# Kernel tuning notes

Hardware: AMD Instinct MI355X
Metric: run time of the kernel (lower is better)

## Reference

```python
import jax, jax.numpy as jnp
import numpy as np

NUM_NODES = 100000
D_IN = 64
D_OUT = 64
NUM_EDGES = 1200000


def setup_inputs() -> dict:
    key = jax.random.key(0)
    k1, k2, k3, k4 = jax.random.split(key, 4)
    features = jax.random.normal(k1, (NUM_NODES, D_IN), dtype=jnp.float32)
    edge_index = jax.random.randint(k2, (2, NUM_EDGES), 0, NUM_NODES, dtype=jnp.int64)
    # Linear(input_dim*2 -> output_dim) parameters
    W = jax.random.normal(k3, (2 * D_IN, D_OUT), dtype=jnp.float32) / np.sqrt(2 * D_IN)
    b = jax.random.normal(k4, (D_OUT,), dtype=jnp.float32) * 0.01
    return {"features": features, "edge_index": edge_index, "W": W, "b": b}


def reference(features, edge_index, W, b):
    num_nodes = features.shape[0]
    src, dst = edge_index[0], edge_index[1]
    # gather source-node features for every edge: [E, D]
    src_feats = features[src]
    # segment-sum into destination nodes (mean aggregation)
    neigh_sum = jax.ops.segment_sum(src_feats, dst, num_segments=num_nodes)
    degree = jax.ops.segment_sum(jnp.ones_like(dst, dtype=features.dtype), dst,
                                 num_segments=num_nodes)
    degree = jnp.clip(degree, 1.0)
    neigh_mean = neigh_sum / degree[:, None]
    # concat self + neighbor features, then linear (dropout = identity in eval)
    combined = jnp.concatenate([features, neigh_mean], axis=-1)
    return combined @ W + b
```

## Files before the change

kernel.cpp:

```cpp
#include <hip/hip_runtime.h>
#include <hip/hip_fp8.h>

#define N_NODES 100000
#define D 64
#define N_EDGES 1200000
#define NCB 391
#define NBLK 256
#define PAD 16
#define CHUNK ((N_EDGES + NBLK - 1) / NBLK)

typedef __attribute__((ext_vector_type(8))) short short8v;
typedef __attribute__((ext_vector_type(4))) float f32x4;

__device__ __forceinline__ unsigned short f2bf(float x) {
    unsigned int b = __float_as_uint(x);
    b += 0x7FFFu + ((b >> 16) & 1u);
    return (unsigned short)(b >> 16);
}
__device__ __forceinline__ unsigned char ftofp8(float x) {
    __hip_fp8_e4m3 q(x);
    return (unsigned char)q.__x;
}
#if __has_builtin(__builtin_amdgcn_cvt_f32_fp8)
#define F8D(w, s) __builtin_amdgcn_cvt_f32_fp8((w), (s))
#else
__device__ __forceinline__ float f8dec(unsigned int w, unsigned int s) {
    __hip_fp8_e4m3 q; q.__x = (unsigned char)(w >> (8 * s));
    return (float)q;
}
#define F8D(w, s) f8dec((w), (s))
#endif

__global__ __launch_bounds__(256) void bin_hist(
    const int* __restrict__ eidx, int* __restrict__ hist, int* __restrict__ totP,
    const float* __restrict__ feat, unsigned char* __restrict__ f8b,
    const float* __restrict__ W, ushort* __restrict__ wb)
{
    __shared__ int h[NCB];
    for (int i = threadIdx.x; i < NCB; i += 256) h[i] = 0;
    __syncthreads();
    const int blk = blockIdx.x;

    if (blk < 32) {
        int g  = blk * 256 + threadIdx.x;
        int j  = g & 7;
        int l  = (g >> 3) & 63;
        int c4 = (g >> 9) & 3;
        int tt = g >> 11;
        int k   = 32 * tt + ((l >> 4) << 3) + j;
        int col = 16 * c4 + (l & 15);
        wb[g] = f2bf(W[k * 64 + col]);
    }

    const int beg = blk * CHUNK;
    const int end = min(beg + CHUNK, N_EDGES);
    for (int e = beg + threadIdx.x; e < end; e += 256)
        atomicAdd(&h[eidx[N_EDGES + e] >> 8], 1);

    const int total4 = N_NODES * D / 4;
    for (int i = blk * 256 + threadIdx.x; i < total4; i += NBLK * 256) {
        float4 v = ((const float4*)feat)[i];
        uchar4 o;
        o.x = ftofp8(v.x); o.y = ftofp8(v.y); o.z = ftofp8(v.z); o.w = ftofp8(v.w);
        ((uchar4*)f8b)[i] = o;
    }

    __syncthreads();
    for (int i = threadIdx.x; i < NCB; i += 256) {
        int v = h[i];
        hist[blk * NCB + i] = v;
        if (v) atomicAdd(&totP[i * PAD], v);
    }
}

__global__ __launch_bounds__(256) void rstart(
    const int* __restrict__ totP, const int* __restrict__ hist,
    int* __restrict__ boff, int* __restrict__ runstart, int* __restrict__ offs)
{
    __shared__ int red[256];
    __shared__ int pfx[256];
    __shared__ int bo_s;

    const int tid = threadIdx.x;
    const int i   = blockIdx.x;

    int p = 0;
    for (int j = tid; j < i; j += 256) p += totP[j * PAD];
    red[tid] = p;
    __syncthreads();
    for (int off = 128; off > 0; off >>= 1) {
        if (tid < off) red[tid] += red[tid + off];
        __syncthreads();
    }
    if (tid == 0) {
        bo_s = red[0];
        boff[i] = red[0];
        if (i == 0) { boff[NCB] = N_EDGES; offs[N_NODES] = N_EDGES; }
    }
    __syncthreads();

    int v = hist[tid * NCB + i];
    pfx[tid] = v;
    __syncthreads();
    for (int off = 1; off < 256; off <<= 1) {
        int x = (tid >= off) ? pfx[tid - off] : 0;
        __syncthreads();
        pfx[tid] += x;
        __syncthreads();
    }
    runstart[tid * NCB + i] = bo_s + pfx[tid] - v;
}

__global__ __launch_bounds__(256) void bin_fill(
    const int* __restrict__ eidx, const int* __restrict__ runstart,
    unsigned int* __restrict__ pairs)
{
    __shared__ int lcur[NCB];
    const int blk = blockIdx.x;
    for (int i = threadIdx.x; i < NCB; i += 256) lcur[i] = runstart[blk * NCB + i];
    __syncthreads();
    const int beg = blk * CHUNK;
    const int end = min(beg + CHUNK, N_EDGES);
    for (int e = beg + threadIdx.x; e < end; e += 256) {
        int src = eidx[e];
        int dst = eidx[N_EDGES + e];
        int pos = atomicAdd(&lcur[dst >> 8], 1);
        pairs[pos] = ((unsigned int)src << 8) | (unsigned int)(dst & 255);
    }
}

__global__ __launch_bounds__(256) void fine_sort(
    const unsigned int* __restrict__ pairs,
    const int* __restrict__ boff,
    int* __restrict__ offs,
    int* __restrict__ csr)
{
    __shared__ int cnt[256];
    __shared__ int pfx[256];
    __shared__ int lcur[256];

    const int tid = threadIdx.x;
    const int b   = blockIdx.x;
    const int beg = boff[b];
    const int end = boff[b + 1];

    cnt[tid] = 0;
    __syncthreads();
    for (int j = beg + tid; j < end; j += 256)
        atomicAdd(&cnt[pairs[j] & 255], 1);
    __syncthreads();

    int v = cnt[tid];
    pfx[tid] = v;
    __syncthreads();
    for (int off = 1; off < 256; off <<= 1) {
        int x = (tid >= off) ? pfx[tid - off] : 0;
        __syncthreads();
        pfx[tid] += x;
        __syncthreads();
    }
    int ex = pfx[tid] - v;
    lcur[tid] = ex;
    int gn = b * 256 + tid;
    if (gn < N_NODES) offs[gn] = beg + ex;
    __syncthreads();

    for (int j = beg + tid; j < end; j += 256) {
        unsigned int p = pairs[j];
        int pos = beg + atomicAdd(&lcur[p & 255], 1);
        csr[pos] = (int)(p >> 8);
    }
}

#define MROW 72
#define D8X(sel) (((F8D(w0.x,sel)+F8D(w1.x,sel))+(F8D(w2.x,sel)+F8D(w3.x,sel))) \
               + ((F8D(w4.x,sel)+F8D(w5.x,sel))+(F8D(w6.x,sel)+F8D(w7.x,sel))))
#define D8Y(sel) (((F8D(w0.y,sel)+F8D(w1.y,sel))+(F8D(w2.y,sel)+F8D(w3.y,sel))) \
               + ((F8D(w4.y,sel)+F8D(w5.y,sel))+(F8D(w6.y,sel)+F8D(w7.y,sel))))
#define D4X(sel) ((F8D(w0.x,sel)+F8D(w1.x,sel))+(F8D(w2.x,sel)+F8D(w3.x,sel)))
#define D4Y(sel) ((F8D(w0.y,sel)+F8D(w1.y,sel))+(F8D(w2.y,sel)+F8D(w3.y,sel)))
__global__ __launch_bounds__(256) void agg_gemm(
    const unsigned char* __restrict__ f8b,
    const float* __restrict__ feat,
    const int* __restrict__ offs,
    const int* __restrict__ csr,
    const ushort* __restrict__ wb,
    const float* __restrict__ bias,
    float* __restrict__ out)
{
    __shared__ __attribute__((aligned(16))) ushort means[32 * MROW];

    const int tid = threadIdx.x;
    const int n0  = blockIdx.x * 32;

    const int l    = tid & 7;
    const int node = tid >> 3;
    const int n    = n0 + node;

    const int beg = offs[n];
    const int end = offs[n + 1];
    const uint2* g8 = (const uint2*)f8b;

    float s0=0.f,s1=0.f,s2=0.f,s3=0.f,s4=0.f,s5=0.f,s6=0.f,s7=0.f;
    int e = beg;
    for (; e + 8 <= end; e += 8) {
        int i0=csr[e+0], i1=csr[e+1], i2=csr[e+2], i3=csr[e+3];
        int i4=csr[e+4], i5=csr[e+5], i6=csr[e+6], i7=csr[e+7];
        uint2 w0 = g8[(size_t)i0 * 8 + l];
        uint2 w1 = g8[(size_t)i1 * 8 + l];
        uint2 w2 = g8[(size_t)i2 * 8 + l];
        uint2 w3 = g8[(size_t)i3 * 8 + l];
        uint2 w4 = g8[(size_t)i4 * 8 + l];
        uint2 w5 = g8[(size_t)i5 * 8 + l];
        uint2 w6 = g8[(size_t)i6 * 8 + l];
        uint2 w7 = g8[(size_t)i7 * 8 + l];
        s0 += D8X(0); s1 += D8X(1); s2 += D8X(2); s3 += D8X(3);
        s4 += D8Y(0); s5 += D8Y(1); s6 += D8Y(2); s7 += D8Y(3);
    }
    for (; e + 4 <= end; e += 4) {
        int i0=csr[e+0], i1=csr[e+1], i2=csr[e+2], i3=csr[e+3];
        uint2 w0 = g8[(size_t)i0 * 8 + l];
        uint2 w1 = g8[(size_t)i1 * 8 + l];
        uint2 w2 = g8[(size_t)i2 * 8 + l];
        uint2 w3 = g8[(size_t)i3 * 8 + l];
        s0 += D4X(0); s1 += D4X(1); s2 += D4X(2); s3 += D4X(3);
        s4 += D4Y(0); s5 += D4Y(1); s6 += D4Y(2); s7 += D4Y(3);
    }
    for (; e < end; ++e) {
        uint2 w0 = g8[(size_t)csr[e] * 8 + l];
        s0 += F8D(w0.x,0); s1 += F8D(w0.x,1); s2 += F8D(w0.x,2); s3 += F8D(w0.x,3);
        s4 += F8D(w0.y,0); s5 += F8D(w0.y,1); s6 += F8D(w0.y,2); s7 += F8D(w0.y,3);
    }

    float dg = (float)(end - beg);
    dg = dg > 1.0f ? dg : 1.0f;
    float inv = 1.0f / dg;
    {
        ushort s[8] = { f2bf(s0*inv), f2bf(s1*inv), f2bf(s2*inv), f2bf(s3*inv),
                        f2bf(s4*inv), f2bf(s5*inv), f2bf(s6*inv), f2bf(s7*inv) };
        *(ushort4*)(means + node * MROW + l * 8)     = *(ushort4*)&s[0];
        *(ushort4*)(means + node * MROW + l * 8 + 4) = *(ushort4*)&s[4];
    }
    __syncthreads();

    const int lane = tid & 63;
    const int wv   = tid >> 6;
    const int rt   = wv >> 1;
    const int cp   = wv & 1;
    const int kg   = lane >> 4;
    const int cl   = lane & 15;

    const float* frow = feat + (size_t)(n0 + rt * 16 + cl) * 64;
    f32x4 p0 = *(const f32x4*)(frow + kg * 8);
    f32x4 p1 = *(const f32x4*)(frow + kg * 8 + 4);
    f32x4 p2 = *(const f32x4*)(frow + 32 + kg * 8);
    f32x4 p3 = *(const f32x4*)(frow + 32 + kg * 8 + 4);
    short8v a0, a1;
    #pragma unroll
    for (int k = 0; k < 4; ++k) {
        a0[k]     = (short)f2bf(p0[k]);
        a0[k + 4] = (short)f2bf(p1[k]);
        a1[k]     = (short)f2bf(p2[k]);
        a1[k + 4] = (short)f2bf(p3[k]);
    }
    const ushort* mrow = means + (rt * 16 + cl) * MROW;
    short8v a2 = *(const short8v*)(mrow + kg * 8);
    short8v a3 = *(const short8v*)(mrow + 32 + kg * 8);

    const short8v* wv8 = (const short8v*)wb;

    #pragma unroll
    for (int q = 0; q < 2; ++q) {
        const int c4 = cp * 2 + q;
        float bv = bias[c4 * 16 + cl];
        f32x4 acc = (f32x4){bv, bv, bv, bv};
        acc = __builtin_amdgcn_mfma_f32_16x16x32_bf16(
            a0, wv8[(0 * 4 + c4) * 64 + lane], acc, 0, 0, 0);
        acc = __builtin_amdgcn_mfma_f32_16x16x32_bf16(
            a1, wv8[(1 * 4 + c4) * 64 + lane], acc, 0, 0, 0);
        acc = __builtin_amdgcn_mfma_f32_16x16x32_bf16(
            a2, wv8[(2 * 4 + c4) * 64 + lane], acc, 0, 0, 0);
        acc = __builtin_amdgcn_mfma_f32_16x16x32_bf16(
            a3, wv8[(3 * 4 + c4) * 64 + lane], acc, 0, 0, 0);
        #pragma unroll
        for (int r = 0; r < 4; ++r)
            out[(size_t)(n0 + rt * 16 + kg * 4 + r) * 64 + c4 * 16 + cl] = acc[r];
    }
}

extern "C" void kernel_launch(void* const* d_in, const int* in_sizes, int n_in,
                              void* d_out, int out_size, void* d_ws, size_t ws_size,
                              hipStream_t stream) {
    const float* feat = (const float*)d_in[0];
    const int*   eidx = (const int*)d_in[1];
    const float* W    = (const float*)d_in[2];
    const float* bias = (const float*)d_in[3];
    float* out = (float*)d_out;

    int* hist     = (int*)d_ws;
    int* totP     = hist + NBLK * NCB;
    int* runstart = totP + NCB * PAD;
    int* boff     = runstart + NBLK * NCB;
    int* offs     = boff + 396;
    int* csr      = offs + 100004;
    ushort* wb    = (ushort*)(csr + N_EDGES);
    unsigned int* pairs = (unsigned int*)(wb + 8192);
    unsigned char* f8b  = (unsigned char*)(pairs + N_EDGES);

    hipMemsetAsync(totP, 0, (size_t)NCB * PAD * sizeof(int), stream);

    bin_hist<<<NBLK, 256, 0, stream>>>(eidx, hist, totP, feat, f8b, W, wb);
    rstart<<<NCB, 256, 0, stream>>>(totP, hist, boff, runstart, offs);
    bin_fill<<<NBLK, 256, 0, stream>>>(eidx, runstart, pairs);
    fine_sort<<<NCB, 256, 0, stream>>>(pairs, boff, offs, csr);
    agg_gemm<<<N_NODES / 32, 256, 0, stream>>>(f8b, feat, offs, csr, wb, bias, out);
}
```

Before: 89.70 us.

## Fuse fine CSR sort into aggregation kernel with 32-node bins in LDS

Coarse destination bins shrink from 256 to 32 nodes, giving 3125 bins, one per aggregation block. The separate fine_sort kernel and the global CSR/offsets arrays are removed. Each aggregation block now counting-sorts its own bin's pairs into a shared-memory CSR and aggregates from there. This saves a launch and a global CSR write and read. In exchange, the histogram/prefix stages handle about 8x more bins: more totP atomics, a larger hist, and strided hist and runstart accesses. rstart also remaps block order across XCDs and changes runstart to a bin-major layout. Neighbor lists are capped at 2048 per bin in shared memory, so a bin with more edges would be silently truncated.

```diff
diff --git a/kernel.cpp b/kernel.cpp
--- a/kernel.cpp
+++ b/kernel.cpp
@@ -4,10 +4,11 @@
 #define N_NODES 100000
 #define D 64
 #define N_EDGES 1200000
-#define NCB 391
+#define NCB 3125
 #define NBLK 256
 #define PAD 16
 #define CHUNK ((N_EDGES + NBLK - 1) / NBLK)
+#define CSRMAX 2048
 
 typedef __attribute__((ext_vector_type(8))) short short8v;
 typedef __attribute__((ext_vector_type(4))) float f32x4;
@@ -55,7 +56,7 @@
     const int beg = blk * CHUNK;
     const int end = min(beg + CHUNK, N_EDGES);
     for (int e = beg + threadIdx.x; e < end; e += 256)
-        atomicAdd(&h[eidx[N_EDGES + e] >> 8], 1);
+        atomicAdd(&h[eidx[N_EDGES + e] >> 5], 1);
 
     const int total4 = N_NODES * D / 4;
     for (int i = blk * 256 + threadIdx.x; i < total4; i += NBLK * 256) {
@@ -75,14 +76,16 @@
 
 __global__ __launch_bounds__(256) void rstart(
     const int* __restrict__ totP, const int* __restrict__ hist,
-    int* __restrict__ boff, int* __restrict__ runstart, int* __restrict__ offs)
+    int* __restrict__ boff, int* __restrict__ runstart)
 {
     __shared__ int red[256];
     __shared__ int pfx[256];
     __shared__ int bo_s;
 
     const int tid = threadIdx.x;
-    const int i   = blockIdx.x;
+    const int q = NCB / 8, r = NCB % 8;
+    const int xcd = blockIdx.x % 8, idx = blockIdx.x / 8;
+    const int i = (xcd < r ? xcd * (q + 1) : r * (q + 1) + (xcd - r) * q) + idx;
 
     int p = 0;
     for (int j = tid; j < i; j += 256) p += totP[j * PAD];
@@ -95,7 +98,7 @@
     if (tid == 0) {
         bo_s = red[0];
         boff[i] = red[0];
-        if (i == 0) { boff[NCB] = N_EDGES; offs[N_NODES] = N_EDGES; }
+        if (i == 0) boff[NCB] = N_EDGES;
     }
     __syncthreads();
 
@@ -108,7 +111,7 @@
         pfx[tid] += x;
         __syncthreads();
     }
-    runstart[tid * NCB + i] = bo_s + pfx[tid] - v;
+    runstart[i * 256 + tid] = bo_s + pfx[tid] - v;
 }
 
 __global__ __launch_bounds__(256) void bin_fill(
@@ -117,58 +120,15 @@
 {
     __shared__ int lcur[NCB];
     const int blk = blockIdx.x;
-    for (int i = threadIdx.x; i < NCB; i += 256) lcur[i] = runstart[blk * NCB + i];
+    for (int i = threadIdx.x; i < NCB; i += 256) lcur[i] = runstart[i * 256 + blk];
     __syncthreads();
     const int beg = blk * CHUNK;
     const int end = min(beg + CHUNK, N_EDGES);
     for (int e = beg + threadIdx.x; e < end; e += 256) {
         int src = eidx[e];
         int dst = eidx[N_EDGES + e];
-        int pos = atomicAdd(&lcur[dst >> 8], 1);
-        pairs[pos] = ((unsigned int)src << 8) | (unsigned int)(dst & 255);
-    }
-}
-
-__global__ __launch_bounds__(256) void fine_sort(
-    const unsigned int* __restrict__ pairs,
-    const int* __restrict__ boff,
-    int* __restrict__ offs,
-    int* __restrict__ csr)
-{
-    __shared__ int cnt[256];
-    __shared__ int pfx[256];
-    __shared__ int lcur[256];
-
-    const int tid = threadIdx.x;
-    const int b   = blockIdx.x;
-    const int beg = boff[b];
-    const int end = boff[b + 1];
-
-    cnt[tid] = 0;
-    __syncthreads();
-    for (int j = beg + tid; j < end; j += 256)
-        atomicAdd(&cnt[pairs[j] & 255], 1);
-    __syncthreads();
-
-    int v = cnt[tid];
-    pfx[tid] = v;
-    __syncthreads();
-    for (int off = 1; off < 256; off <<= 1) {
-        int x = (tid >= off) ? pfx[tid - off] : 0;
-        __syncthreads();
-        pfx[tid] += x;
-        __syncthreads();
-    }
-    int ex = pfx[tid] - v;
-    lcur[tid] = ex;
-    int gn = b * 256 + tid;
-    if (gn < N_NODES) offs[gn] = beg + ex;
-    __syncthreads();
-
-    for (int j = beg + tid; j < end; j += 256) {
-        unsigned int p = pairs[j];
-        int pos = beg + atomicAdd(&lcur[p & 255], 1);
-        csr[pos] = (int)(p >> 8);
+        int pos = atomicAdd(&lcur[dst >> 5], 1);
+        pairs[pos] = ((unsigned int)src << 5) | (unsigned int)(dst & 31);
     }
 }
 
@@ -179,33 +139,63 @@
                + ((F8D(w4.y,sel)+F8D(w5.y,sel))+(F8D(w6.y,sel)+F8D(w7.y,sel))))
 #define D4X(sel) ((F8D(w0.x,sel)+F8D(w1.x,sel))+(F8D(w2.x,sel)+F8D(w3.x,sel)))
 #define D4Y(sel) ((F8D(w0.y,sel)+F8D(w1.y,sel))+(F8D(w2.y,sel)+F8D(w3.y,sel)))
-__global__ __launch_bounds__(256) void agg_gemm(
+__global__ __launch_bounds__(256) void sage_fused(
     const unsigned char* __restrict__ f8b,
     const float* __restrict__ feat,
-    const int* __restrict__ offs,
-    const int* __restrict__ csr,
+    const int* __restrict__ boff,
+    const unsigned int* __restrict__ pairs,
     const ushort* __restrict__ wb,
     const float* __restrict__ bias,
     float* __restrict__ out)
 {
+    __shared__ int cnt[32];
+    __shared__ int lofs[33];
+    __shared__ int lcur2[32];
+    __shared__ int csrL[CSRMAX];
     __shared__ __attribute__((aligned(16))) ushort means[32 * MROW];
 
     const int tid = threadIdx.x;
-    const int n0  = blockIdx.x * 32;
+    const int b   = blockIdx.x;
+    const int n0  = b * 32;
+    const int beg = boff[b];
+    const int end = boff[b + 1];
+
+    if (tid < 32) cnt[tid] = 0;
+    __syncthreads();
+    for (int j = beg + tid; j < end; j += 256)
+        atomicAdd(&cnt[pairs[j] & 31], 1);
+    __syncthreads();
+    if (tid == 0) {
+        int run = 0;
+        #pragma unroll
+        for (int k = 0; k < 32; ++k) { lofs[k] = run; run += cnt[k]; }
+        lofs[32] = run;
+    }
+    __syncthreads();
+    if (tid < 32) lcur2[tid] = lofs[tid];
+    __syncthreads();
+    for (int j = beg + tid; j < end; j += 256) {
+        unsigned int p = pairs[j];
+        int pos = atomicAdd(&lcur2[p & 31], 1);
+        if (pos < CSRMAX) csrL[pos] = (int)(p >> 5);
+    }
+    __syncthreads();
 
     const int l    = tid & 7;
     const int node = tid >> 3;
-    const int n    = n0 + node;
-
-    const int beg = offs[n];
-    const int end = offs[n + 1];
+
+    int ebeg = lofs[node];
+    int eend = lofs[node + 1];
+    const int deg = eend - ebeg;
+    if (ebeg > CSRMAX) ebeg = CSRMAX;
+    if (eend > CSRMAX) eend = CSRMAX;
     const uint2* g8 = (const uint2*)f8b;
 
     float s0=0.f,s1=0.f,s2=0.f,s3=0.f,s4=0.f,s5=0.f,s6=0.f,s7=0.f;
-    int e = beg;
-    for (; e + 8 <= end; e += 8) {
-        int i0=csr[e+0], i1=csr[e+1], i2=csr[e+2], i3=csr[e+3];
-        int i4=csr[e+4], i5=csr[e+5], i6=csr[e+6], i7=csr[e+7];
+    int e = ebeg;
+    for (; e + 8 <= eend; e += 8) {
+        int i0=csrL[e+0], i1=csrL[e+1], i2=csrL[e+2], i3=csrL[e+3];
+        int i4=csrL[e+4], i5=csrL[e+5], i6=csrL[e+6], i7=csrL[e+7];
         uint2 w0 = g8[(size_t)i0 * 8 + l];
         uint2 w1 = g8[(size_t)i1 * 8 + l];
         uint2 w2 = g8[(size_t)i2 * 8 + l];
@@ -217,8 +207,8 @@
         s0 += D8X(0); s1 += D8X(1); s2 += D8X(2); s3 += D8X(3);
         s4 += D8Y(0); s5 += D8Y(1); s6 += D8Y(2); s7 += D8Y(3);
     }
-    for (; e + 4 <= end; e += 4) {
-        int i0=csr[e+0], i1=csr[e+1], i2=csr[e+2], i3=csr[e+3];
+    for (; e + 4 <= eend; e += 4) {
+        int i0=csrL[e+0], i1=csrL[e+1], i2=csrL[e+2], i3=csrL[e+3];
         uint2 w0 = g8[(size_t)i0 * 8 + l];
         uint2 w1 = g8[(size_t)i1 * 8 + l];
         uint2 w2 = g8[(size_t)i2 * 8 + l];
@@ -226,13 +216,13 @@
         s0 += D4X(0); s1 += D4X(1); s2 += D4X(2); s3 += D4X(3);
         s4 += D4Y(0); s5 += D4Y(1); s6 += D4Y(2); s7 += D4Y(3);
     }
-    for (; e < end; ++e) {
-        uint2 w0 = g8[(size_t)csr[e] * 8 + l];
+    for (; e < eend; ++e) {
+        uint2 w0 = g8[(size_t)csrL[e] * 8 + l];
         s0 += F8D(w0.x,0); s1 += F8D(w0.x,1); s2 += F8D(w0.x,2); s3 += F8D(w0.x,3);
         s4 += F8D(w0.y,0); s5 += F8D(w0.y,1); s6 += F8D(w0.y,2); s7 += F8D(w0.y,3);
     }
 
-    float dg = (float)(end - beg);
+    float dg = (float)deg;
     dg = dg > 1.0f ? dg : 1.0f;
     float inv = 1.0f / dg;
     {
@@ -270,8 +260,8 @@
     const short8v* wv8 = (const short8v*)wb;
 
     #pragma unroll
-    for (int q = 0; q < 2; ++q) {
-        const int c4 = cp * 2 + q;
+    for (int qq = 0; qq < 2; ++qq) {
+        const int c4 = cp * 2 + qq;
         float bv = bias[c4 * 16 + cl];
         f32x4 acc = (f32x4){bv, bv, bv, bv};
         acc = __builtin_amdgcn_mfma_f32_16x16x32_bf16(
@@ -300,18 +290,15 @@
     int* hist     = (int*)d_ws;
     int* totP     = hist + NBLK * NCB;
     int* runstart = totP + NCB * PAD;
-    int* boff     = runstart + NBLK * NCB;
-    int* offs     = boff + 396;
-    int* csr      = offs + 100004;
-    ushort* wb    = (ushort*)(csr + N_EDGES);
+    int* boff     = runstart + NCB * 256;
+    ushort* wb    = (ushort*)(boff + 3128);
     unsigned int* pairs = (unsigned int*)(wb + 8192);
     unsigned char* f8b  = (unsigned char*)(pairs + N_EDGES);
 
     hipMemsetAsync(totP, 0, (size_t)NCB * PAD * sizeof(int), stream);
 
     bin_hist<<<NBLK, 256, 0, stream>>>(eidx, hist, totP, feat, f8b, W, wb);
-    rstart<<<NCB, 256, 0, stream>>>(totP, hist, boff, runstart, offs);
+    rstart<<<NCB, 256, 0, stream>>>(totP, hist, boff, runstart);
     bin_fill<<<NBLK, 256, 0, stream>>>(eidx, runstart, pairs);
-    fine_sort<<<NCB, 256, 0, stream>>>(pairs, boff, offs, csr);
-    agg_gemm<<<N_NODES / 32, 256, 0, stream>>>(f8b, feat, offs, csr, wb, bias, out);
-}
+    sage_fused<<<NCB, 256, 0, stream>>>(f8b, feat, boff, pairs, wb, bias, out);
+}
```

Result: slower. 131.1 us (+46.1%).
